# Kernel tuning notes

Measured on AMD Instinct MI355X. Metric: run time of the kernel, lower is better.

The kernel has to match this reference:

```python
import jax, jax.numpy as jnp
import numpy as np

D_MODEL = 1024
N_HEAD = 16
D_K = 64
D_V = 64
SEQ = 4096


def setup_inputs() -> dict:
    key = jax.random.key(0)
    ks = jax.random.split(key, 7)
    s = 1.0 / np.sqrt(D_MODEL)
    return {
        "q": jax.random.normal(ks[0], (SEQ, D_MODEL), dtype=jnp.float32),
        "k": jax.random.normal(ks[1], (SEQ, D_MODEL), dtype=jnp.float32),
        "v": jax.random.normal(ks[2], (SEQ, D_MODEL), dtype=jnp.float32),
        "Wq": jax.random.normal(ks[3], (N_HEAD * D_K, D_MODEL), dtype=jnp.float32) * s,
        "Wk": jax.random.normal(ks[4], (N_HEAD * D_K, D_MODEL), dtype=jnp.float32) * s,
        "Wv": jax.random.normal(ks[5], (N_HEAD * D_V, D_MODEL), dtype=jnp.float32) * s,
        "Wfc": jax.random.normal(ks[6], (D_MODEL, N_HEAD * D_V), dtype=jnp.float32) * s,
    }


def reference(q, k, v, Wq, Wk, Wv, Wfc):
    len_q = q.shape[0]
    residual = q
    temperature = jnp.asarray(np.sqrt(D_K), q.dtype)
    # projections: [len, n_head, d_k] -> [n_head, len, d_k]
    qh = (q @ Wq.T).reshape(len_q, N_HEAD, D_K).transpose(1, 0, 2)
    kh = (k @ Wk.T).reshape(k.shape[0], N_HEAD, D_K).transpose(1, 0, 2)
    vh = (v @ Wv.T).reshape(v.shape[0], N_HEAD, D_V).transpose(1, 0, 2)
    # scores: [n_head, len_q, len_k]
    attn = jnp.einsum('hqd,hkd->hqk', qh / temperature, kh)
    attn = jax.nn.softmax(attn, axis=-1)  # dropout = identity (eval)
    out = jnp.einsum('hqk,hkd->hqd', attn, vh)  # [n_head, len_q, d_v]
    out = out.transpose(1, 0, 2).reshape(len_q, N_HEAD * D_V)
    out = out @ Wfc.T  # dropout = identity (eval)
    return jax.nn.relu(out) + residual
```

## Files before the change

### kernel.cpp

```cpp
#include <hip/hip_runtime.h>
#include <math.h>

#define SEQ    4096
#define DMODEL 1024
#define NHEAD  16
#define DHEAD  64

typedef __bf16 bf16;
typedef bf16  bf16x2 __attribute__((ext_vector_type(2)));
typedef bf16  bf16x4 __attribute__((ext_vector_type(4)));
typedef bf16  bf16x8 __attribute__((ext_vector_type(8)));
typedef float f32x4  __attribute__((ext_vector_type(4)));
typedef float f32x16 __attribute__((ext_vector_type(16)));
typedef unsigned int u32;

#define SWZ(r)  ((((r) >> 2) ^ (r)) & 7)
#define SWZ3(r) (((r) ^ ((r) >> 2) ^ ((r) >> 3)) & 7)

__device__ __forceinline__ void gll16(const void* g, void* l) {
    __builtin_amdgcn_global_load_lds(
        (const __attribute__((address_space(1))) void*)g,
        (__attribute__((address_space(3))) void*)l, 16, 0, 0);
}

__device__ __forceinline__ u32 cvtpk(float lo, float hi) {
    u32 r;
    asm("v_cvt_pk_bf16_f32 %0, %1, %2" : "=v"(r) : "v"(lo), "v"(hi));
    return r;
}
__device__ __forceinline__ void pswap(u32& a, u32& b) {
    asm volatile("v_permlane32_swap_b32 %0, %1" : "+v"(a), "+v"(b));
}

__global__ __launch_bounds__(256)
void cvt_bf16(const float* __restrict__ s, bf16* __restrict__ d, int n)
{
    const int i = (blockIdx.x * 256 + threadIdx.x) * 8;
    if (i >= n) return;
    float4 a = *(const float4*)&s[i];
    float4 b = *(const float4*)&s[i + 4];
    bf16x8 v;
    v[0] = (bf16)a.x; v[1] = (bf16)a.y; v[2] = (bf16)a.z; v[3] = (bf16)a.w;
    v[4] = (bf16)b.x; v[5] = (bf16)b.y; v[6] = (bf16)b.z; v[7] = (bf16)b.w;
    *(bf16x8*)&d[i] = v;
}

template<int EPI>
__global__ __launch_bounds__(256)
void gemm_mfma(const bf16* __restrict__ A, const bf16* __restrict__ B,
               bf16* __restrict__ Cb, float* __restrict__ Cf,
               const float* __restrict__ res, int M, int N, int K)
{
    const int bm   = blockIdx.y * 64;
    const int bn   = blockIdx.x * 128;
    const int tid  = threadIdx.x;
    const int w    = tid >> 6;
    const int lane = tid & 63;
    const int lr   = lane & 15;
    const int lh   = lane >> 4;
    const int wr   = w >> 1;
    const int wc   = w & 1;
    const int lrow = lane >> 3;
    const int lch  = lane & 7;

    __shared__ bf16 As[64 * 64];
    __shared__ bf16 Bs[128 * 64];

    f32x4 acc[2][4] = {};

    for (int k0 = 0; k0 < K; k0 += 64) {
        __syncthreads();
        #pragma unroll
        for (int i = 0; i < 2; ++i) {
            const int r = (w * 2 + i) * 8 + lrow;
            gll16(A + (size_t)(bm + r) * K + k0 + ((lch ^ SWZ(r)) << 3),
                  &As[(w * 2 + i) * 512]);
        }
        #pragma unroll
        for (int i = 0; i < 4; ++i) {
            const int r = (w * 4 + i) * 8 + lrow;
            gll16(B + (size_t)(bn + r) * K + k0 + ((lch ^ SWZ(r)) << 3),
                  &Bs[(w * 4 + i) * 512]);
        }
        asm volatile("s_waitcnt vmcnt(0)" ::: "memory");
        __syncthreads();

        bf16x8 af[2][2], bfr[4][2];
        #pragma unroll
        for (int rt = 0; rt < 2; ++rt)
            #pragma unroll
            for (int s = 0; s < 2; ++s) {
                const int r = wr * 32 + rt * 16 + lr;
                af[rt][s] = *(const bf16x8*)&As[r * 64 + (((s * 4 + lh) ^ SWZ(r)) << 3)];
            }
        #pragma unroll
        for (int ct = 0; ct < 4; ++ct)
            #pragma unroll
            for (int s = 0; s < 2; ++s) {
                const int r = wc * 64 + ct * 16 + lr;
                bfr[ct][s] = *(const bf16x8*)&Bs[r * 64 + (((s * 4 + lh) ^ SWZ(r)) << 3)];
            }
        __builtin_amdgcn_s_setprio(1);
        #pragma unroll
        for (int rt = 0; rt < 2; ++rt)
            #pragma unroll
            for (int ct = 0; ct < 4; ++ct)
                #pragma unroll
                for (int s = 0; s < 2; ++s)
                    acc[rt][ct] = __builtin_amdgcn_mfma_f32_16x16x32_bf16(
                        af[rt][s], bfr[ct][s], acc[rt][ct], 0, 0, 0);
        __builtin_amdgcn_s_setprio(0);
    }

    #pragma unroll
    for (int rt = 0; rt < 2; ++rt)
        #pragma unroll
        for (int ct = 0; ct < 4; ++ct)
            #pragma unroll
            for (int r = 0; r < 4; ++r) {
                const int m = bm + wr * 32 + rt * 16 + lh * 4 + r;
                const int n = bn + wc * 64 + ct * 16 + lr;
                if (EPI == 0) {
                    Cb[(size_t)m * N + n] = (bf16)acc[rt][ct][r];
                } else {
                    Cf[(size_t)m * N + n] =
                        fmaxf(acc[rt][ct][r], 0.f) + res[(size_t)m * N + n];
                }
            }
}

__global__ __launch_bounds__(256)
void attn_mfma(const bf16* __restrict__ Q, const bf16* __restrict__ K,
               const bf16* __restrict__ V, bf16* __restrict__ O)
{
    const int wg   = blockIdx.x;
    const int swz  = (wg & 7) * 64 + (wg >> 3);
    const int h    = swz >> 5;
    const int q0   = (swz & 31) * 128;

    const int tid  = threadIdx.x;
    const int w    = tid >> 6;
    const int lane = tid & 63;
    const int lo5  = lane & 31;
    const int hi   = lane >> 5;
    const int lrow = lane >> 3;
    const int lch  = lane & 7;

    __shared__ bf16 Ks[2][64 * 64];
    __shared__ bf16 Vt[2][64 * 64];

    const bf16* qrow = Q + (size_t)(q0 + w * 32 + lo5) * DMODEL + h * 64;
    bf16x8 qf[4];
    #pragma unroll
    for (int s = 0; s < 4; ++s)
        qf[s] = *(const bf16x8*)&qrow[s * 16 + hi * 8];

    f32x16 acc0 = {}, acc1 = {};
    float ls0 = 0.f, ls1 = 0.f;

    const int vk = (tid & 7) * 8;
    const int vd = (tid >> 3) * 2;

    const float SC = 0.18033688f;

    #pragma unroll
    for (int i = 0; i < 2; ++i) {
        const int r = (w * 2 + i) * 8 + lrow;
        gll16(K + (size_t)r * DMODEL + h * 64 + ((lch ^ SWZ3(r)) << 3),
              &Ks[0][(w * 2 + i) * 512]);
    }
    {
        bf16x2 u[8];
        #pragma unroll
        for (int i = 0; i < 8; ++i)
            u[i] = *(const bf16x2*)&V[(size_t)(vk + i) * DMODEL + h * 64 + vd];
        asm volatile("s_waitcnt vmcnt(0)" ::: "memory");
        bf16x8 v0, v1;
        #pragma unroll
        for (int i = 0; i < 8; ++i) { v0[i] = u[i][0]; v1[i] = u[i][1]; }
        *(bf16x8*)&Vt[0][(vd + 0) * 64 + (((tid & 7) ^ SWZ3(vd + 0)) << 3)] = v0;
        *(bf16x8*)&Vt[0][(vd + 1) * 64 + (((tid & 7) ^ SWZ3(vd + 1)) << 3)] = v1;
    }
    __syncthreads();

#define BODY(CUR, CN)                                                          \
    {                                                                          \
        const int cn = (CN) & (SEQ - 1);                                       \
                               \
        _Pragma("unroll")                                                      \
        for (int i = 0; i < 2; ++i) {                                          \
            const int r = (w * 2 + i) * 8 + lrow;                              \
            gll16(K + (size_t)(cn + r) * DMODEL + h * 64 + ((lch ^ SWZ3(r)) << 3), \
                  &Ks[(CUR) ^ 1][(w * 2 + i) * 512]);                          \
        }                                                                      \
        bf16x2 u[8];                                                           \
        _Pragma("unroll")                                                      \
        for (int i = 0; i < 8; ++i)                                            \
            u[i] = *(const bf16x2*)&V[(size_t)(cn + vk + i) * DMODEL + h * 64 + vd]; \
                                                \
        const bf16* Kc = Ks[CUR];                                              \
        f32x16 st0 = {}, st1 = {};                                             \
        __builtin_amdgcn_s_setprio(1);                                         \
        _Pragma("unroll")                                                      \
        for (int s = 0; s < 4; ++s) {                                          \
            const int r0 = lo5, r1 = 32 + lo5;                                 \
            bf16x8 kf0 = *(const bf16x8*)&Kc[r0 * 64 + (((s * 2 + hi) ^ SWZ3(r0)) << 3)]; \
            bf16x8 kf1 = *(const bf16x8*)&Kc[r1 * 64 + (((s * 2 + hi) ^ SWZ3(r1)) << 3)]; \
            st0 = __builtin_amdgcn_mfma_f32_32x32x16_bf16(kf0, qf[s], st0, 0, 0, 0); \
            st1 = __builtin_amdgcn_mfma_f32_32x32x16_bf16(kf1, qf[s], st1, 0, 0, 0); \
        }                                                                      \
        __builtin_amdgcn_s_setprio(0);                                         \
                                            \
        float p[32];                                                           \
        float a0 = 0.f, a1 = 0.f, a2 = 0.f, a3 = 0.f;                          \
        _Pragma("unroll")                                                      \
        for (int r = 0; r < 16; ++r) {                                         \
            float s0 = fminf(st0[r] * SC, 50.f);                               \
            float s1 = fminf(st1[r] * SC, 50.f);                               \
            p[r]      = __builtin_amdgcn_exp2f(s0);                            \
            p[16 + r] = __builtin_amdgcn_exp2f(s1);                            \
            if (r & 1) { a1 += p[r]; a3 += p[16 + r]; }                        \
            else       { a0 += p[r]; a2 += p[16 + r]; }                        \
        }                                                                      \
        ls0 += a0 + a1; ls1 += a2 + a3;                                        \
                          \
        union { u32 wd[4]; bf16x8 v; } fr[4];                                  \
        _Pragma("unroll")                                                      \
        for (int ks = 0; ks < 4; ++ks) {                                       \
            const int b = (ks & 1) * 8 + (ks >> 1) * 16;                       \
            u32 A0 = cvtpk(p[b + 0], p[b + 1]);                                \
            u32 C0 = cvtpk(p[b + 2], p[b + 3]);                                \
            u32 B0 = cvtpk(p[b + 4], p[b + 5]);                                \
            u32 D0 = cvtpk(p[b + 6], p[b + 7]);                                \
            pswap(A0, B0);                                                     \
            pswap(C0, D0);                                                     \
            fr[ks].wd[0] = A0; fr[ks].wd[1] = C0;                              \
            fr[ks].wd[2] = B0; fr[ks].wd[3] = D0;                              \
        }                                                                      \
                                                     \
        const bf16* Vc = Vt[CUR];                                              \
        __builtin_amdgcn_s_setprio(1);                                         \
        _Pragma("unroll")                                                      \
        for (int ks = 0; ks < 4; ++ks) {                                       \
            const int r0 = lo5, r1 = 32 + lo5;                                 \
            bf16x8 vf0 = *(const bf16x8*)&Vc[r0 * 64 + (((ks * 2 + hi) ^ SWZ3(r0)) << 3)]; \
            bf16x8 vf1 = *(const bf16x8*)&Vc[r1 * 64 + (((ks * 2 + hi) ^ SWZ3(r1)) << 3)]; \
            acc0 = __builtin_amdgcn_mfma_f32_32x32x16_bf16(vf0, fr[ks].v, acc0, 0, 0, 0); \
            acc1 = __builtin_amdgcn_mfma_f32_32x32x16_bf16(vf1, fr[ks].v, acc1, 0, 0, 0); \
        }                                                                      \
        __builtin_amdgcn_s_setprio(0);                                         \
                        \
        asm volatile("s_waitcnt vmcnt(0)" ::: "memory");                       \
        {                                                                      \
            bf16x8 v0, v1;                                                     \
            _Pragma("unroll")                                                  \
            for (int i = 0; i < 8; ++i) { v0[i] = u[i][0]; v1[i] = u[i][1]; }  \
            bf16* Vn = Vt[(CUR) ^ 1];                                          \
            *(bf16x8*)&Vn[(vd + 0) * 64 + (((tid & 7) ^ SWZ3(vd + 0)) << 3)] = v0; \
            *(bf16x8*)&Vn[(vd + 1) * 64 + (((tid & 7) ^ SWZ3(vd + 1)) << 3)] = v1; \
        }                                                                      \
        __syncthreads();                                                       \
    }

    for (int c = 0; c < SEQ; c += 128) {
        BODY(0, c + 64)
        BODY(1, c + 128)
    }
#undef BODY

    float lt = ls0 + ls1;
    lt += __shfl_xor(lt, 32);
    const float inv = 1.0f / lt;

    bf16* orow = O + (size_t)(q0 + w * 32 + lo5) * DMODEL + h * 64;
    #pragma unroll
    for (int g = 0; g < 4; ++g) {
        bf16x4 o4;
        o4[0] = (bf16)(acc0[g * 4 + 0] * inv);
        o4[1] = (bf16)(acc0[g * 4 + 1] * inv);
        o4[2] = (bf16)(acc0[g * 4 + 2] * inv);
        o4[3] = (bf16)(acc0[g * 4 + 3] * inv);
        *(bf16x4*)&orow[g * 8 + 4 * hi] = o4;
        bf16x4 o5;
        o5[0] = (bf16)(acc1[g * 4 + 0] * inv);
        o5[1] = (bf16)(acc1[g * 4 + 1] * inv);
        o5[2] = (bf16)(acc1[g * 4 + 2] * inv);
        o5[3] = (bf16)(acc1[g * 4 + 3] * inv);
        *(bf16x4*)&orow[32 + g * 8 + 4 * hi] = o5;
    }
}

extern "C" void kernel_launch(void* const* d_in, const int* in_sizes, int n_in,
                              void* d_out, int out_size, void* d_ws, size_t ws_size,
                              hipStream_t stream)
{
    const float* q   = (const float*)d_in[0];
    const float* k   = (const float*)d_in[1];
    const float* v   = (const float*)d_in[2];
    const float* Wq  = (const float*)d_in[3];
    const float* Wk  = (const float*)d_in[4];
    const float* Wv  = (const float*)d_in[5];
    const float* Wfc = (const float*)d_in[6];
    float* out = (float*)d_out;

    const int EM = SEQ * DMODEL;
    const int WM = DMODEL * DMODEL;

    bf16* qb   = (bf16*)d_ws;
    bf16* kb   = qb + EM;
    bf16* vb   = kb + EM;
    bf16* Wqb  = vb + EM;
    bf16* Wkb  = Wqb + WM;
    bf16* Wvb  = Wkb + WM;
    bf16* Wfcb = Wvb + WM;
    bf16* Pq   = Wfcb + WM;
    bf16* Pk   = Pq + EM;
    bf16* Pv   = Pk + EM;
    bf16* AO   = Pv + EM;

    cvt_bf16<<<EM / 2048, 256, 0, stream>>>(q,   qb,   EM);
    cvt_bf16<<<EM / 2048, 256, 0, stream>>>(k,   kb,   EM);
    cvt_bf16<<<EM / 2048, 256, 0, stream>>>(v,   vb,   EM);
    cvt_bf16<<<WM / 2048, 256, 0, stream>>>(Wq,  Wqb,  WM);
    cvt_bf16<<<WM / 2048, 256, 0, stream>>>(Wk,  Wkb,  WM);
    cvt_bf16<<<WM / 2048, 256, 0, stream>>>(Wv,  Wvb,  WM);
    cvt_bf16<<<WM / 2048, 256, 0, stream>>>(Wfc, Wfcb, WM);

    dim3 gg(DMODEL / 128, SEQ / 64);
    gemm_mfma<0><<<gg, 256, 0, stream>>>(qb, Wqb, Pq, nullptr, nullptr, SEQ, DMODEL, DMODEL);
    gemm_mfma<0><<<gg, 256, 0, stream>>>(kb, Wkb, Pk, nullptr, nullptr, SEQ, DMODEL, DMODEL);
    gemm_mfma<0><<<gg, 256, 0, stream>>>(vb, Wvb, Pv, nullptr, nullptr, SEQ, DMODEL, DMODEL);

    attn_mfma<<<512, 256, 0, stream>>>(Pq, Pk, Pv, AO);

    gemm_mfma<1><<<gg, 256, 0, stream>>>(AO, Wfcb, nullptr, out, q, SEQ, DMODEL, DMODEL);
}
```

Before: 219.4 us.

## Split attention KV range into halves with combine kernel; shrink GEMM tiles

The attention kernel now splits the key/value sequence into two halves. This doubles the workgroup count to 1024, and each workgroup writes an unnormalised partial output plus its row sums. A new combine kernel adds the two partial outputs and divides by the summed denominators. The projection GEMMs use 64x64 output tiles instead of 64x128 to launch twice as many blocks. Both changes aim for better CU occupancy, at the cost of an extra pass over partial outputs and less operand reuse per GEMM block.

```diff
diff --git a/kernel.cpp b/kernel.cpp
--- a/kernel.cpp
+++ b/kernel.cpp
@@ -5,6 +5,7 @@
 #define DMODEL 1024
 #define NHEAD  16
 #define DHEAD  64
+#define KVHALF 2048
 
 typedef __bf16 bf16;
 typedef bf16  bf16x2 __attribute__((ext_vector_type(2)));
@@ -52,7 +53,7 @@
                const float* __restrict__ res, int M, int N, int K)
 {
     const int bm   = blockIdx.y * 64;
-    const int bn   = blockIdx.x * 128;
+    const int bn   = blockIdx.x * 64;
     const int tid  = threadIdx.x;
     const int w    = tid >> 6;
     const int lane = tid & 63;
@@ -64,9 +65,9 @@
     const int lch  = lane & 7;
 
     __shared__ bf16 As[64 * 64];
-    __shared__ bf16 Bs[128 * 64];
-
-    f32x4 acc[2][4] = {};
+    __shared__ bf16 Bs[64 * 64];
+
+    f32x4 acc[2][2] = {};
 
     for (int k0 = 0; k0 < K; k0 += 64) {
         __syncthreads();
@@ -77,15 +78,15 @@
                   &As[(w * 2 + i) * 512]);
         }
         #pragma unroll
-        for (int i = 0; i < 4; ++i) {
-            const int r = (w * 4 + i) * 8 + lrow;
+        for (int i = 0; i < 2; ++i) {
+            const int r = (w * 2 + i) * 8 + lrow;
             gll16(B + (size_t)(bn + r) * K + k0 + ((lch ^ SWZ(r)) << 3),
-                  &Bs[(w * 4 + i) * 512]);
+                  &Bs[(w * 2 + i) * 512]);
         }
         asm volatile("s_waitcnt vmcnt(0)" ::: "memory");
         __syncthreads();
 
-        bf16x8 af[2][2], bfr[4][2];
+        bf16x8 af[2][2], bfr[2][2];
         #pragma unroll
         for (int rt = 0; rt < 2; ++rt)
             #pragma unroll
@@ -94,17 +95,17 @@
                 af[rt][s] = *(const bf16x8*)&As[r * 64 + (((s * 4 + lh) ^ SWZ(r)) << 3)];
             }
         #pragma unroll
-        for (int ct = 0; ct < 4; ++ct)
+        for (int ct = 0; ct < 2; ++ct)
             #pragma unroll
             for (int s = 0; s < 2; ++s) {
-                const int r = wc * 64 + ct * 16 + lr;
+                const int r = wc * 32 + ct * 16 + lr;
                 bfr[ct][s] = *(const bf16x8*)&Bs[r * 64 + (((s * 4 + lh) ^ SWZ(r)) << 3)];
             }
         __builtin_amdgcn_s_setprio(1);
         #pragma unroll
         for (int rt = 0; rt < 2; ++rt)
             #pragma unroll
-            for (int ct = 0; ct < 4; ++ct)
+            for (int ct = 0; ct < 2; ++ct)
                 #pragma unroll
                 for (int s = 0; s < 2; ++s)
                     acc[rt][ct] = __builtin_amdgcn_mfma_f32_16x16x32_bf16(
@@ -115,11 +116,11 @@
     #pragma unroll
     for (int rt = 0; rt < 2; ++rt)
         #pragma unroll
-        for (int ct = 0; ct < 4; ++ct)
+        for (int ct = 0; ct < 2; ++ct)
             #pragma unroll
             for (int r = 0; r < 4; ++r) {
                 const int m = bm + wr * 32 + rt * 16 + lh * 4 + r;
-                const int n = bn + wc * 64 + ct * 16 + lr;
+                const int n = bn + wc * 32 + ct * 16 + lr;
                 if (EPI == 0) {
                     Cb[(size_t)m * N + n] = (bf16)acc[rt][ct][r];
                 } else {
@@ -131,12 +132,19 @@
 
 __global__ __launch_bounds__(256)
 void attn_mfma(const bf16* __restrict__ Q, const bf16* __restrict__ K,
-               const bf16* __restrict__ V, bf16* __restrict__ O)
+               const bf16* __restrict__ V,
+               bf16* __restrict__ Oa, bf16* __restrict__ Ob,
+               float* __restrict__ La, float* __restrict__ Lb)
 {
     const int wg   = blockIdx.x;
-    const int swz  = (wg & 7) * 64 + (wg >> 3);
-    const int h    = swz >> 5;
-    const int q0   = (swz & 31) * 128;
+    const int lgc  = (wg & 7) * 128 + (wg >> 3);
+    const int half = lgc >> 9;
+    const int h    = (lgc >> 5) & 15;
+    const int q0   = (lgc & 31) * 128;
+    const int c0   = half * KVHALF;
+
+    bf16*  Op = half ? Ob : Oa;
+    float* Lp = half ? Lb : La;
 
     const int tid  = threadIdx.x;
     const int w    = tid >> 6;
@@ -166,14 +174,14 @@
     #pragma unroll
     for (int i = 0; i < 2; ++i) {
         const int r = (w * 2 + i) * 8 + lrow;
-        gll16(K + (size_t)r * DMODEL + h * 64 + ((lch ^ SWZ3(r)) << 3),
+        gll16(K + (size_t)(c0 + r) * DMODEL + h * 64 + ((lch ^ SWZ3(r)) << 3),
               &Ks[0][(w * 2 + i) * 512]);
     }
     {
         bf16x2 u[8];
         #pragma unroll
         for (int i = 0; i < 8; ++i)
-            u[i] = *(const bf16x2*)&V[(size_t)(vk + i) * DMODEL + h * 64 + vd];
+            u[i] = *(const bf16x2*)&V[(size_t)(c0 + vk + i) * DMODEL + h * 64 + vd];
         asm volatile("s_waitcnt vmcnt(0)" ::: "memory");
         bf16x8 v0, v1;
         #pragma unroll
@@ -185,8 +193,7 @@
 
 #define BODY(CUR, CN)                                                          \
     {                                                                          \
-        const int cn = (CN) & (SEQ - 1);                                       \
-                               \
+        const int cn = c0 + (((CN) - c0) & (KVHALF - 1));                      \
         _Pragma("unroll")                                                      \
         for (int i = 0; i < 2; ++i) {                                          \
             const int r = (w * 2 + i) * 8 + lrow;                              \
@@ -197,7 +204,6 @@
         _Pragma("unroll")                                                      \
         for (int i = 0; i < 8; ++i)                                            \
             u[i] = *(const bf16x2*)&V[(size_t)(cn + vk + i) * DMODEL + h * 64 + vd]; \
-                                                \
         const bf16* Kc = Ks[CUR];                                              \
         f32x16 st0 = {}, st1 = {};                                             \
         __builtin_amdgcn_s_setprio(1);                                         \
@@ -210,7 +216,6 @@
             st1 = __builtin_amdgcn_mfma_f32_32x32x16_bf16(kf1, qf[s], st1, 0, 0, 0); \
         }                                                                      \
         __builtin_amdgcn_s_setprio(0);                                         \
-                                            \
         float p[32];                                                           \
         float a0 = 0.f, a1 = 0.f, a2 = 0.f, a3 = 0.f;                          \
         _Pragma("unroll")                                                      \
@@ -223,7 +228,6 @@
             else       { a0 += p[r]; a2 += p[16 + r]; }                        \
         }                                                                      \
         ls0 += a0 + a1; ls1 += a2 + a3;                                        \
-                          \
         union { u32 wd[4]; bf16x8 v; } fr[4];                                  \
         _Pragma("unroll")                                                      \
         for (int ks = 0; ks < 4; ++ks) {                                       \
@@ -237,7 +241,6 @@
             fr[ks].wd[0] = A0; fr[ks].wd[1] = C0;                              \
             fr[ks].wd[2] = B0; fr[ks].wd[3] = D0;                              \
         }                                                                      \
-                                                     \
         const bf16* Vc = Vt[CUR];                                              \
         __builtin_amdgcn_s_setprio(1);                                         \
         _Pragma("unroll")                                                      \
@@ -249,7 +252,6 @@
             acc1 = __builtin_amdgcn_mfma_f32_32x32x16_bf16(vf1, fr[ks].v, acc1, 0, 0, 0); \
         }                                                                      \
         __builtin_amdgcn_s_setprio(0);                                         \
-                        \
         asm volatile("s_waitcnt vmcnt(0)" ::: "memory");                       \
         {                                                                      \
             bf16x8 v0, v1;                                                     \
@@ -262,7 +264,7 @@
         __syncthreads();                                                       \
     }
 
-    for (int c = 0; c < SEQ; c += 128) {
+    for (int c = c0; c < c0 + KVHALF; c += 128) {
         BODY(0, c + 64)
         BODY(1, c + 128)
     }
@@ -270,24 +272,42 @@
 
     float lt = ls0 + ls1;
     lt += __shfl_xor(lt, 32);
-    const float inv = 1.0f / lt;
-
-    bf16* orow = O + (size_t)(q0 + w * 32 + lo5) * DMODEL + h * 64;
+    Lp[h * SEQ + q0 + w * 32 + lo5] = lt;
+
+    bf16* orow = Op + (size_t)(q0 + w * 32 + lo5) * DMODEL + h * 64;
     #pragma unroll
     for (int g = 0; g < 4; ++g) {
         bf16x4 o4;
-        o4[0] = (bf16)(acc0[g * 4 + 0] * inv);
-        o4[1] = (bf16)(acc0[g * 4 + 1] * inv);
-        o4[2] = (bf16)(acc0[g * 4 + 2] * inv);
-        o4[3] = (bf16)(acc0[g * 4 + 3] * inv);
+        o4[0] = (bf16)acc0[g * 4 + 0];
+        o4[1] = (bf16)acc0[g * 4 + 1];
+        o4[2] = (bf16)acc0[g * 4 + 2];
+        o4[3] = (bf16)acc0[g * 4 + 3];
         *(bf16x4*)&orow[g * 8 + 4 * hi] = o4;
         bf16x4 o5;
-        o5[0] = (bf16)(acc1[g * 4 + 0] * inv);
-        o5[1] = (bf16)(acc1[g * 4 + 1] * inv);
-        o5[2] = (bf16)(acc1[g * 4 + 2] * inv);
-        o5[3] = (bf16)(acc1[g * 4 + 3] * inv);
+        o5[0] = (bf16)acc1[g * 4 + 0];
+        o5[1] = (bf16)acc1[g * 4 + 1];
+        o5[2] = (bf16)acc1[g * 4 + 2];
+        o5[3] = (bf16)acc1[g * 4 + 3];
         *(bf16x4*)&orow[32 + g * 8 + 4 * hi] = o5;
     }
+}
+
+__global__ __launch_bounds__(256)
+void combine(const bf16* __restrict__ Oa, const bf16* __restrict__ Ob,
+             const float* __restrict__ La, const float* __restrict__ Lb,
+             bf16* __restrict__ AO)
+{
+    const int e   = (blockIdx.x * 256 + threadIdx.x) * 8;
+    const int row = e >> 10;
+    const int hh  = (e >> 6) & 15;
+    const float inv = 1.0f / (La[hh * SEQ + row] + Lb[hh * SEQ + row]);
+    bf16x8 a = *(const bf16x8*)&Oa[e];
+    bf16x8 b = *(const bf16x8*)&Ob[e];
+    bf16x8 o;
+    #pragma unroll
+    for (int i = 0; i < 8; ++i)
+        o[i] = (bf16)(((float)a[i] + (float)b[i]) * inv);
+    *(bf16x8*)&AO[e] = o;
 }
 
 extern "C" void kernel_launch(void* const* d_in, const int* in_sizes, int n_in,
@@ -306,17 +326,22 @@
     const int EM = SEQ * DMODEL;
     const int WM = DMODEL * DMODEL;
 
-    bf16* qb   = (bf16*)d_ws;
+    bf16* Wfcb = (bf16*)d_ws;
+    bf16* qb   = Wfcb + WM;
     bf16* kb   = qb + EM;
     bf16* vb   = kb + EM;
     bf16* Wqb  = vb + EM;
     bf16* Wkb  = Wqb + WM;
     bf16* Wvb  = Wkb + WM;
-    bf16* Wfcb = Wvb + WM;
-    bf16* Pq   = Wfcb + WM;
+    bf16* Pq   = Wvb + WM;
     bf16* Pk   = Pq + EM;
     bf16* Pv   = Pk + EM;
     bf16* AO   = Pv + EM;
+
+    bf16*  Oa = qb;
+    bf16*  Ob = kb;
+    float* La = (float*)vb;
+    float* Lb = La + NHEAD * SEQ;
 
     cvt_bf16<<<EM / 2048, 256, 0, stream>>>(q,   qb,   EM);
     cvt_bf16<<<EM / 2048, 256, 0, stream>>>(k,   kb,   EM);
@@ -326,12 +351,14 @@
     cvt_bf16<<<WM / 2048, 256, 0, stream>>>(Wv,  Wvb,  WM);
     cvt_bf16<<<WM / 2048, 256, 0, stream>>>(Wfc, Wfcb, WM);
 
-    dim3 gg(DMODEL / 128, SEQ / 64);
+    dim3 gg(DMODEL / 64, SEQ / 64);
     gemm_mfma<0><<<gg, 256, 0, stream>>>(qb, Wqb, Pq, nullptr, nullptr, SEQ, DMODEL, DMODEL);
     gemm_mfma<0><<<gg, 256, 0, stream>>>(kb, Wkb, Pk, nullptr, nullptr, SEQ, DMODEL, DMODEL);
     gemm_mfma<0><<<gg, 256, 0, stream>>>(vb, Wvb, Pv, nullptr, nullptr, SEQ, DMODEL, DMODEL);
 
-    attn_mfma<<<512, 256, 0, stream>>>(Pq, Pk, Pv, AO);
+    attn_mfma<<<1024, 256, 0, stream>>>(Pq, Pk, Pv, Oa, Ob, La, Lb);
+
+    combine<<<EM / 2048, 256, 0, stream>>>(Oa, Ob, La, Lb, AO);
 
     gemm_mfma<1><<<gg, 256, 0, stream>>>(AO, Wfcb, nullptr, out, q, SEQ, DMODEL, DMODEL);
 }
```

Result: no change. 221.1 us (+0.8%).
